# Kernel tuning notes

Hardware: AMD Instinct MI355X
Metric: run time of the kernel (lower is better)

## Reference

```python
import jax, jax.numpy as jnp
import numpy as np

NR_HEADS = 8


def segment_softmax(scores, indices, num_segments):
    # numerically stable softmax within each segment
    seg_max = jax.ops.segment_max(scores, indices, num_segments=num_segments)
    e = jnp.exp(scores - seg_max[indices])
    denom = jax.ops.segment_sum(e, indices, num_segments=num_segments)
    return e / denom[indices]


def setup_inputs() -> dict:
    key = jax.random.key(0)
    ks = jax.random.split(key, 10)
    n_ast, d, n_cfg = 500000, 128, 32768
    H, combined = NR_HEADS, 128
    w_scale = 1.0 / np.sqrt(d)
    return {
        "ast_nodes_encodings": jax.random.normal(ks[0], (n_ast, d), jnp.float32),
        "Wq": jax.random.normal(ks[1], (H, d, d), jnp.float32) * w_scale,
        "bq": jnp.zeros((H, d), jnp.float32),
        "Wk": jax.random.normal(ks[2], (H, d, d), jnp.float32) * w_scale,
        "bk": jnp.zeros((H, d), jnp.float32),
        "Wo": jax.random.normal(ks[3], (H * d, combined), jnp.float32) * (1.0 / np.sqrt(H * d)),
        "bo": jnp.zeros((combined,), jnp.float32),
        "ast_key": jax.random.randint(ks[4], (n_ast,), 0, n_ast, jnp.int32),
        "ast_value": jax.random.randint(ks[5], (n_ast,), 0, n_cfg, jnp.int32),
        "pdg_key": jnp.arange(n_cfg, dtype=jnp.int32),
        "pdg_value": jax.random.randint(ks[6], (n_cfg,), 0, n_ast, jnp.int32),
        "nr_cfg_nodes": n_cfg,
    }


def reference(ast_nodes_encodings, Wq, bq, Wk, bk, Wo, bo,
              ast_key, ast_value, pdg_key, pdg_value, nr_cfg_nodes):
    N = int(nr_cfg_nodes)
    d = ast_nodes_encodings.shape[1]
    inv_sqrt_d = 1.0 / np.sqrt(d)

    # Build per-PDG-node attention queries: gather sub-AST root encodings, scatter into [N, d]
    root_encodings = ast_nodes_encodings[pdg_value]                   # [N_map, d]
    attn_queries = jnp.zeros((N, d), ast_nodes_encodings.dtype).at[pdg_key].set(root_encodings)

    # Gather scattered inputs (one row per AST node assigned to a PDG node)
    values = ast_nodes_encodings[ast_key]                              # [E, d]
    indices = ast_value                                                # [E]

    # Multi-head scatter attention (ScatterCombiner with combining_method='attn')
    head_outs = []
    for h in range(NR_HEADS):  # small fixed head count; avoids [E, H, d] intermediates
        q = attn_queries @ Wq[h] + bq[h]                               # [N, d]
        k = values @ Wk[h] + bk[h]                                     # [E, d]
        scores = jnp.sum(q[indices] * k, axis=-1) * inv_sqrt_d         # [E]
        probs = segment_softmax(scores, indices, N)                    # [E]
        head_outs.append(jax.ops.segment_sum(probs[:, None] * values, indices, num_segments=N))

    combined = jnp.concatenate(head_outs, axis=-1) @ Wo + bo           # [N, combined_dim]
    return combined
```

## Files before the change

kernel.cpp:

```cpp
#include <hip/hip_runtime.h>
#include <hip/hip_bf16.h>
#include <cstdint>

typedef __hip_bfloat16 bf16;
typedef unsigned int uint;
typedef unsigned short ushort;

#define DEVI __device__ __forceinline__

DEVI float blo(uint u){ return __uint_as_float(u << 16); }
DEVI float bhi(uint u){ return __uint_as_float(u & 0xffff0000u); }
DEVI ushort f2b(float x){ uint u = __float_as_uint(x); uint r = (u + 0x7fffu + ((u >> 16) & 1u)) >> 16; return (ushort)r; }
DEVI uint pack2(float a, float b){ return (uint)f2b(a) | ((uint)f2b(b) << 16); }
DEVI float b2f(ushort h){ return __uint_as_float((uint)h << 16); }

typedef short bf16x8 __attribute__((ext_vector_type(8)));
typedef float f32x4  __attribute__((ext_vector_type(4)));

DEVI float row16_sum(float x){
  int y;
  y = __builtin_amdgcn_update_dpp(0, __float_as_int(x), 0x121, 0xF, 0xF, true); x += __int_as_float(y);
  y = __builtin_amdgcn_update_dpp(0, __float_as_int(x), 0x122, 0xF, 0xF, true); x += __int_as_float(y);
  y = __builtin_amdgcn_update_dpp(0, __float_as_int(x), 0x124, 0xF, 0xF, true); x += __int_as_float(y);
  y = __builtin_amdgcn_update_dpp(0, __float_as_int(x), 0x128, 0xF, 0xF, true); x += __int_as_float(y);
  return x;
}

__global__ __launch_bounds__(256) void build_M(const float* __restrict__ Wq, const float* __restrict__ Wk,
                                               float* __restrict__ Mb){
  __shared__ float WkL[128*33];
  __shared__ float WqL[16*33];
  const int t = threadIdx.x;
  const int h = blockIdx.x >> 3, pg = blockIdx.x & 7, p0 = pg*16;
  const float* wk = Wk + (size_t)h*16384;
  const float* wq = Wq + ((size_t)h*128 + p0)*128;
  const int m = t & 127, half = t >> 7;
  float acc[8] = {0,0,0,0,0,0,0,0};
  for (int jc = 0; jc < 4; ++jc){
    __syncthreads();
    #pragma unroll
    for (int i = 0; i < 4; ++i){
      int g = t + 256*i;
      int mm = g >> 3, j0 = (g & 7)*4;
      float4 v = *(const float4*)(wk + mm*128 + jc*32 + j0);
      float* d = &WkL[mm*33 + j0];
      d[0] = v.x; d[1] = v.y; d[2] = v.z; d[3] = v.w;
    }
    {
      int e = t*2;
      int pr = e >> 5, jj = e & 31;
      float2 v = *(const float2*)(wq + pr*128 + jc*32 + jj);
      WqL[pr*33 + jj] = v.x; WqL[pr*33 + jj + 1] = v.y;
    }
    __syncthreads();
    for (int j = 0; j < 32; ++j){
      float wkv = WkL[m*33 + j];
      #pragma unroll
      for (int r = 0; r < 8; ++r)
        acc[r] = fmaf(WqL[(half*8 + r)*33 + j], wkv, acc[r]);
    }
  }
  #pragma unroll
  for (int r = 0; r < 8; ++r)
    Mb[(size_t)(p0 + half*8 + r)*1024 + h*128 + m] = acc[r];
}

__global__ void build_bias(const float* __restrict__ Wq, const float* __restrict__ Wk,
                           const float* __restrict__ bq, const float* __restrict__ bk,
                           float* __restrict__ cvec, float* __restrict__ uvec, float* __restrict__ sv){
  int h = blockIdx.x, m = threadIdx.x;
  const float* wkr = Wk + ((size_t)h*128 + m)*128;
  const float* wqr = Wq + ((size_t)h*128 + m)*128;
  const float* bqr = bq + h*128;
  const float* bkr = bk + h*128;
  float c = 0.f, u = 0.f;
  for (int j = 0; j < 128; ++j){
    c = fmaf(wkr[j], bqr[j], c);
    u = fmaf(wqr[j], bkr[j], u);
  }
  cvec[h*128 + m] = c;
  uvec[h*128 + m] = u;
  if (m == 0){
    float s = 0.f;
    for (int j = 0; j < 128; ++j) s = fmaf(bqr[j], bkr[j], s);
    sv[h] = s;
  }
}

__global__ void scatter_aq(const int* __restrict__ pk, const int* __restrict__ pv,
                           const float* __restrict__ ast, float* __restrict__ aq,
                           ushort* __restrict__ aqh, ushort* __restrict__ aql, int n_map){
  int i = blockIdx.x;
  if (i >= n_map) return;
  int k = pk[i], src = pv[i];
  int lane = threadIdx.x;
  float2 v = *(const float2*)(ast + (size_t)src*128 + 2*lane);
  *(float2*)(aq + (size_t)k*128 + 2*lane) = v;
  ushort h0 = f2b(v.x), h1 = f2b(v.y);
  ushort l0 = f2b(v.x - b2f(h0)), l1 = f2b(v.y - b2f(h1));
  *(uint*)(aqh + (size_t)k*128 + 2*lane) = (uint)h0 | ((uint)h1 << 16);
  *(uint*)(aql + (size_t)k*128 + 2*lane) = (uint)l0 | ((uint)l1 << 16);
}

__global__ void frag_pack(const float* __restrict__ S, uint4* __restrict__ D, int C, int ctn){
  const int b = blockIdx.x;
  const int ks = b / ctn, ct = b - ks*ctn;
  const int l = threadIdx.x;
  const int kb = ks*32 + (l >> 4)*8;
  const int c  = ct*16 + (l & 15);
  ushort hi[8], lo[8];
  #pragma unroll
  for (int j = 0; j < 8; ++j){
    float wv = S[(size_t)(kb + j)*C + c];
    ushort hh = f2b(wv);
    hi[j] = hh;
    lo[j] = f2b(wv - b2f(hh));
  }
  uint4 H, L;
  H.x = (uint)hi[0] | ((uint)hi[1] << 16);
  H.y = (uint)hi[2] | ((uint)hi[3] << 16);
  H.z = (uint)hi[4] | ((uint)hi[5] << 16);
  H.w = (uint)hi[6] | ((uint)hi[7] << 16);
  L.x = (uint)lo[0] | ((uint)lo[1] << 16);
  L.y = (uint)lo[2] | ((uint)lo[3] << 16);
  L.z = (uint)lo[4] | ((uint)lo[5] << 16);
  L.w = (uint)lo[6] | ((uint)lo[7] << 16);
  D[((size_t)b*2 + 0)*64 + l] = H;
  D[((size_t)b*2 + 1)*64 + l] = L;
}

__global__ __launch_bounds__(256, 1) void qt_mfma(const ushort* __restrict__ aqh, const ushort* __restrict__ aql,
                                                  const uint4* __restrict__ Mp, const float* __restrict__ cvec,
                                                  bf16* __restrict__ qt, int N){
  const int l = threadIdx.x & 63, w = threadIdx.x >> 6;
  const int lr = l & 15, lk = l >> 4;
  const int r0 = blockIdx.x*128 + w*32;
  int ra = r0 + lr;      if (ra > N-1) ra = N-1;
  int rb = r0 + 16 + lr; if (rb > N-1) rb = N-1;

  bf16x8 Ah0[4], Al0[4], Ah1[4], Al1[4];
  #pragma unroll
  for (int ks = 0; ks < 4; ++ks){
    Ah0[ks] = *(const bf16x8*)(aqh + (size_t)ra*128 + lk*8 + ks*32);
    Al0[ks] = *(const bf16x8*)(aql + (size_t)ra*128 + lk*8 + ks*32);
    Ah1[ks] = *(const bf16x8*)(aqh + (size_t)rb*128 + lk*8 + ks*32);
    Al1[ks] = *(const bf16x8*)(aql + (size_t)rb*128 + lk*8 + ks*32);
  }
  const uint4* pw = Mp + l;

  bf16x8 Ba[8], Bb[8];
  auto LDB = [&](int ct, bf16x8* B){
    #pragma unroll
    for (int ks = 0; ks < 4; ++ks){
      const uint4* q = pw + ((size_t)(ks*64 + ct)*2)*64;
      B[ks*2]   = *(const bf16x8*)q;
      B[ks*2+1] = *(const bf16x8*)(q + 64);
    }
  };
  auto DO = [&](int ct, bf16x8* B){
    f32x4 a0 = {0.f,0.f,0.f,0.f}, a1 = {0.f,0.f,0.f,0.f};
    #pragma unroll
    for (int ks = 0; ks < 4; ++ks){
      a0 = __builtin_amdgcn_mfma_f32_16x16x32_bf16(Ah0[ks], B[2*ks],   a0, 0, 0, 0);
      a1 = __builtin_amdgcn_mfma_f32_16x16x32_bf16(Ah1[ks], B[2*ks],   a1, 0, 0, 0);
      a0 = __builtin_amdgcn_mfma_f32_16x16x32_bf16(Al0[ks], B[2*ks],   a0, 0, 0, 0);
      a1 = __builtin_amdgcn_mfma_f32_16x16x32_bf16(Al1[ks], B[2*ks],   a1, 0, 0, 0);
      a0 = __builtin_amdgcn_mfma_f32_16x16x32_bf16(Ah0[ks], B[2*ks+1], a0, 0, 0, 0);
      a1 = __builtin_amdgcn_mfma_f32_16x16x32_bf16(Ah1[ks], B[2*ks+1], a1, 0, 0, 0);
    }
    const int cc = ct*16 + lr;
    const float bv = cvec[cc];
    #pragma unroll
    for (int i = 0; i < 4; ++i){
      int rr0 = r0 + lk*4 + i;
      if (rr0 < N) ((ushort*)qt)[(size_t)rr0*1024 + cc] = f2b(a0[i] + bv);
      int rr1 = r0 + 16 + lk*4 + i;
      if (rr1 < N) ((ushort*)qt)[(size_t)rr1*1024 + cc] = f2b(a1[i] + bv);
    }
  };

  LDB(0, Ba);
  for (int ct = 0; ct < 64; ct += 2){
    LDB(ct + 1, Bb);
    DO(ct, Ba);
    if (ct + 2 < 64) LDB(ct + 2, Ba);
    DO(ct + 1, Bb);
  }
}

__global__ void qb_kernel(const float* __restrict__ aq, const float* __restrict__ uvec,
                          const float* __restrict__ sv, float* __restrict__ qb){
  int n = blockIdx.x, lane = threadIdx.x;
  int h = lane >> 3, g = lane & 7;
  const float* ar = aq + (size_t)n*128 + g*16;
  const float* ur = uvec + h*128 + g*16;
  float dot = 0.f;
  #pragma unroll
  for (int k = 0; k < 16; ++k) dot = fmaf(ar[k], ur[k], dot);
  dot += __shfl_xor(dot, 1);
  dot += __shfl_xor(dot, 2);
  dot += __shfl_xor(dot, 4);
  if (g == 0) qb[(size_t)n*8 + h] = dot + sv[h];
}

__global__ void count_edges(const int* __restrict__ av, int* __restrict__ counts, int E){
  int e = blockIdx.x*256 + threadIdx.x;
  if (e < E) atomicAdd(&counts[av[e]], 1);
}

__global__ void scan_offsets(const int* __restrict__ counts, int* __restrict__ offsets, int N){
  __shared__ int pa[1024];
  __shared__ int pb[1024];
  int t = threadIdx.x;
  int CH = (N + 1023) >> 10;
  int b = t*CH, e = b + CH;
  if (b > N) b = N;
  if (e > N) e = N;
  int s = 0;
  for (int i = b; i < e; ++i) s += counts[i];
  pa[t] = s;
  __syncthreads();
  int* src = pa; int* dst = pb;
  for (int off = 1; off < 1024; off <<= 1){
    int v = src[t];
    if (t >= off) v += src[t - off];
    __syncthreads();
    dst[t] = v;
    __syncthreads();
    int* tmp = src; src = dst; dst = tmp;
  }
  int run = src[t] - s;
  for (int i = b; i < e; ++i){ offsets[i] = run; run += counts[i]; }
  if (t == 1023) offsets[N] = src[1023];
}

__global__ void fill_edges(const int* __restrict__ av, const int* __restrict__ akey,
                           const int* __restrict__ offsets, int* __restrict__ cursor,
                           int* __restrict__ ridx, int E){
  int e = blockIdx.x*256 + threadIdx.x;
  if (e < E){
    int seg = av[e];
    int pos = offsets[seg] + atomicAdd(&cursor[seg], 1);
    ridx[pos] = akey[e];
  }
}

__global__ __launch_bounds__(256) void seg_attn(
    const bf16* __restrict__ qt, const float* __restrict__ qb,
    const int* __restrict__ offsets, const int* __restrict__ ridx,
    const float* __restrict__ ast, bf16* __restrict__ ho, int N)
{
  const int wid  = threadIdx.x >> 6;
  const int lane = threadIdx.x & 63;
  const int n = blockIdx.x*4 + wid;
  if (n >= N) return;
  const int beg = __builtin_amdgcn_readfirstlane(offsets[n]);
  const int end = __builtin_amdgcn_readfirstlane(offsets[n+1]);
  const int deg = end - beg;
  const int grp = lane >> 4, d4 = lane & 15;
  const int h0 = 2*grp, h1 = 2*grp + 1;

  const ushort* qtp = (const ushort*)qt + (size_t)n*1024 + d4*8;
  const uint4 Qa = *(const uint4*)(qtp + h0*128);
  const uint4 Qb = *(const uint4*)(qtp + h1*128);
  const float4 q0lo = make_float4(blo(Qa.x), bhi(Qa.x), blo(Qa.y), bhi(Qa.y));
  const float4 q0hi = make_float4(blo(Qa.z), bhi(Qa.z), blo(Qa.w), bhi(Qa.w));
  const float4 q1lo = make_float4(blo(Qb.x), bhi(Qb.x), blo(Qb.y), bhi(Qb.y));
  const float4 q1hi = make_float4(blo(Qb.z), bhi(Qb.z), blo(Qb.w), bhi(Qb.w));
  const float SC = 0.12751744886681336f;
  const float qs0 = qb[(size_t)n*8 + h0] * SC;
  const float qs1 = qb[(size_t)n*8 + h1] * SC;

  const int* rp = ridx + beg;

  float den0 = 0.f, den1 = 0.f;
  float4 x0lo = make_float4(0,0,0,0), x0hi = x0lo, x1lo = x0lo, x1hi = x0lo;

  if (deg > 0){
#define LOADP(Pa0, Pa1, Pb0, Pb1, base) do { \
    int iA = (base) < deg ? (base) : deg-1; \
    int iB = (base)+1 < deg ? (base)+1 : deg-1; \
    const float4* pA = (const float4*)(ast + (size_t)rp[iA]*128 + d4*8); \
    const float4* pB = (const float4*)(ast + (size_t)rp[iB]*128 + d4*8); \
    Pa0 = pA[0]; Pa1 = pA[1]; Pb0 = pB[0]; Pb1 = pB[1]; } while(0)

#define C1(A0, A1) do { \
    float s0, s1; \
    s0 = A0.x*q0lo.x; s0 = fmaf(A0.y, q0lo.y, s0); s0 = fmaf(A0.z, q0lo.z, s0); s0 = fmaf(A0.w, q0lo.w, s0); \
    s0 = fmaf(A1.x, q0hi.x, s0); s0 = fmaf(A1.y, q0hi.y, s0); s0 = fmaf(A1.z, q0hi.z, s0); s0 = fmaf(A1.w, q0hi.w, s0); \
    s1 = A0.x*q1lo.x; s1 = fmaf(A0.y, q1lo.y, s1); s1 = fmaf(A0.z, q1lo.z, s1); s1 = fmaf(A0.w, q1lo.w, s1); \
    s1 = fmaf(A1.x, q1hi.x, s1); s1 = fmaf(A1.y, q1hi.y, s1); s1 = fmaf(A1.z, q1hi.z, s1); s1 = fmaf(A1.w, q1hi.w, s1); \
    s0 = row16_sum(s0); s1 = row16_sum(s1); \
    const float p0 = exp2f(fmaf(s0, SC, qs0)); \
    const float p1 = exp2f(fmaf(s1, SC, qs1)); \
    den0 += p0; den1 += p1; \
    x0lo.x = fmaf(p0, A0.x, x0lo.x); x0lo.y = fmaf(p0, A0.y, x0lo.y); \
    x0lo.z = fmaf(p0, A0.z, x0lo.z); x0lo.w = fmaf(p0, A0.w, x0lo.w); \
    x0hi.x = fmaf(p0, A1.x, x0hi.x); x0hi.y = fmaf(p0, A1.y, x0hi.y); \
    x0hi.z = fmaf(p0, A1.z, x0hi.z); x0hi.w = fmaf(p0, A1.w, x0hi.w); \
    x1lo.x = fmaf(p1, A0.x, x1lo.x); x1lo.y = fmaf(p1, A0.y, x1lo.y); \
    x1lo.z = fmaf(p1, A0.z, x1lo.z); x1lo.w = fmaf(p1, A0.w, x1lo.w); \
    x1hi.x = fmaf(p1, A1.x, x1hi.x); x1hi.y = fmaf(p1, A1.y, x1hi.y); \
    x1hi.z = fmaf(p1, A1.z, x1hi.z); x1hi.w = fmaf(p1, A1.w, x1hi.w); \
  } while(0)

    float4 P0a0, P0a1, P0b0, P0b1;
    float4 P1a0, P1a1, P1b0, P1b1;
    float4 P2a0, P2a1, P2b0, P2b1;
    LOADP(P0a0, P0a1, P0b0, P0b1, 0);
    LOADP(P1a0, P1a1, P1b0, P1b1, 2);
    LOADP(P2a0, P2a1, P2b0, P2b1, 4);
    int e = 0;
    for (; e + 5 < deg; e += 6){
      C1(P0a0, P0a1); C1(P0b0, P0b1); LOADP(P0a0, P0a1, P0b0, P0b1, e + 6);
      C1(P1a0, P1a1); C1(P1b0, P1b1); LOADP(P1a0, P1a1, P1b0, P1b1, e + 8);
      C1(P2a0, P2a1); C1(P2b0, P2b1); LOADP(P2a0, P2a1, P2b0, P2b1, e + 10);
    }
    const int t = deg - e;
    if (t >= 1) C1(P0a0, P0a1);
    if (t >= 2) C1(P0b0, P0b1);
    if (t >= 3) C1(P1a0, P1a1);
    if (t >= 4) C1(P1b0, P1b1);
    if (t >= 5) C1(P2a0, P2a1);
    if (t >= 6) C1(P2b0, P2b1);
#undef C1
#undef LOADP
  }
  const float r0v = (deg > 0) ? (1.f / den0) : 0.f;
  const float r1v = (deg > 0) ? (1.f / den1) : 0.f;

  uint4 o0, o1;
  o0.x = pack2(x0lo.x*r0v, x0lo.y*r0v); o0.y = pack2(x0lo.z*r0v, x0lo.w*r0v);
  o0.z = pack2(x0hi.x*r0v, x0hi.y*r0v); o0.w = pack2(x0hi.z*r0v, x0hi.w*r0v);
  o1.x = pack2(x1lo.x*r1v, x1lo.y*r1v); o1.y = pack2(x1lo.z*r1v, x1lo.w*r1v);
  o1.z = pack2(x1hi.x*r1v, x1hi.y*r1v); o1.w = pack2(x1hi.z*r1v, x1hi.w*r1v);
  ushort* hb = (ushort*)ho + (size_t)n*1024 + d4*8;
  *(uint4*)(hb + h0*128) = o0;
  *(uint4*)(hb + h1*128) = o1;
}

__global__ __launch_bounds__(256, 1) void out_mfma(const bf16* __restrict__ ho, const uint4* __restrict__ Wp,
                                                   const float* __restrict__ bo, float* __restrict__ out, int N){
  const int l = threadIdx.x & 63, w = threadIdx.x >> 6;
  const int lr = l & 15, lk = l >> 4;
  const int r0 = blockIdx.x*128 + w*32;
  int ra = r0 + lr;      if (ra > N-1) ra = N-1;
  int rb = r0 + 16 + lr; if (rb > N-1) rb = N-1;
  const bf16* pa = ho + (size_t)ra*1024 + lk*8;
  const bf16* pb = ho + (size_t)rb*1024 + lk*8;
  const uint4* pw = Wp + l;

  f32x4 acc[2][8];
  #pragma unroll
  for (int i = 0; i < 2; ++i)
    #pragma unroll
    for (int c = 0; c < 8; ++c)
      #pragma unroll
      for (int j = 0; j < 4; ++j) acc[i][c][j] = 0.f;

  bf16x8 Aa[2], Ab[2], Ba[16], Bb[16];

  auto LD = [&](int ks, bf16x8* A, bf16x8* B){
    A[0] = *(const bf16x8*)(pa + ks*32);
    A[1] = *(const bf16x8*)(pb + ks*32);
    const uint4* q = pw + (size_t)ks*1024;
    #pragma unroll
    for (int u = 0; u < 16; ++u) B[u] = *(const bf16x8*)(q + (size_t)u*64);
  };
  auto MM = [&](bf16x8* A, bf16x8* B){
    #pragma unroll
    for (int c = 0; c < 8; ++c){
      acc[0][c] = __builtin_amdgcn_mfma_f32_16x16x32_bf16(A[0], B[2*c],   acc[0][c], 0, 0, 0);
      acc[1][c] = __builtin_amdgcn_mfma_f32_16x16x32_bf16(A[1], B[2*c],   acc[1][c], 0, 0, 0);
      acc[0][c] = __builtin_amdgcn_mfma_f32_16x16x32_bf16(A[0], B[2*c+1], acc[0][c], 0, 0, 0);
      acc[1][c] = __builtin_amdgcn_mfma_f32_16x16x32_bf16(A[1], B[2*c+1], acc[1][c], 0, 0, 0);
    }
  };

  LD(0, Aa, Ba);
  for (int ks = 0; ks < 32; ks += 2){
    LD(ks + 1, Ab, Bb);
    MM(Aa, Ba);
    if (ks + 2 < 32) LD(ks + 2, Aa, Ba);
    MM(Ab, Bb);
  }

  #pragma unroll
  for (int c = 0; c < 8; ++c){
    float bv = bo[c*16 + lr];
    #pragma unroll
    for (int rt = 0; rt < 2; ++rt){
      #pragma unroll
      for (int i = 0; i < 4; ++i){
        int rr = r0 + rt*16 + lk*4 + i;
        if (rr < N) out[(size_t)rr*128 + c*16 + lr] = acc[rt][c][i] + bv;
      }
    }
  }
}

extern "C" void kernel_launch(void* const* d_in, const int* in_sizes, int n_in,
                              void* d_out, int out_size, void* d_ws, size_t ws_size,
                              hipStream_t stream) {
  const float* ast = (const float*)d_in[0];
  const float* Wq  = (const float*)d_in[1];
  const float* bq  = (const float*)d_in[2];
  const float* Wk  = (const float*)d_in[3];
  const float* bk  = (const float*)d_in[4];
  const float* Wo  = (const float*)d_in[5];
  const float* bo  = (const float*)d_in[6];
  const int* ast_key   = (const int*)d_in[7];
  const int* ast_value = (const int*)d_in[8];
  const int* pdg_key   = (const int*)d_in[9];
  const int* pdg_value = (const int*)d_in[10];
  const int E     = in_sizes[7];
  const int n_map = in_sizes[9];
  const int N     = out_size / 128;
  float* out = (float*)d_out;

  char* w = (char*)d_ws;
  auto carve = [&](size_t bytes)->char*{
    char* p = w; w += (bytes + 255) & ~size_t(255); return p;
  };
  bf16*  qt      = (bf16*) carve((size_t)N*1024*2);
  float* aq      = (float*)carve((size_t)N*128*4);
  float* Mb      = (float*)carve((size_t)128*1024*4);
  float* cvec    = (float*)carve(1024*4);
  float* uvec    = (float*)carve(1024*4);
  float* sv      = (float*)carve(8*4);
  float* qb      = (float*)carve((size_t)N*8*4);
  int*   counts  = (int*)  carve((size_t)N*4);
  int*   offsets = (int*)  carve((size_t)(N+1)*4);
  int*   cursor  = (int*)  carve((size_t)N*4);
  int*   ridx    = (int*)  carve((size_t)E*4);
  bf16*  ho      = (bf16*) carve((size_t)N*1024*2);
  uint4* Wp      = (uint4*)carve((size_t)256*2*64*16);
  ushort* aqh    = (ushort*)carve((size_t)N*128*2);
  ushort* aql    = (ushort*)carve((size_t)N*128*2);
  uint4* Mp      = (uint4*)carve((size_t)256*2*64*16);
  (void)ws_size; (void)n_in;

  hipMemsetAsync(aq,     0, (size_t)N*128*4, stream);
  hipMemsetAsync(aqh,    0, (size_t)N*128*2, stream);
  hipMemsetAsync(aql,    0, (size_t)N*128*2, stream);
  hipMemsetAsync(counts, 0, (size_t)N*4, stream);
  hipMemsetAsync(cursor, 0, (size_t)N*4, stream);

  build_M   <<<64, 256, 0, stream>>>(Wq, Wk, Mb);
  build_bias<<<8, 128, 0, stream>>>(Wq, Wk, bq, bk, cvec, uvec, sv);
  frag_pack <<<256, 64, 0, stream>>>(Wo, Wp, 128, 8);
  scatter_aq<<<n_map, 64, 0, stream>>>(pdg_key, pdg_value, ast, aq, aqh, aql, n_map);
  frag_pack <<<256, 64, 0, stream>>>(Mb, Mp, 1024, 64);
  qt_mfma   <<<(N + 127)/128, 256, 0, stream>>>(aqh, aql, Mp, cvec, qt, N);
  qb_kernel <<<N, 64, 0, stream>>>(aq, uvec, sv, qb);
  count_edges<<<(E + 255)/256, 256, 0, stream>>>(ast_value, counts, E);
  scan_offsets<<<1, 1024, 0, stream>>>(counts, offsets, N);
  fill_edges<<<(E + 255)/256, 256, 0, stream>>>(ast_value, ast_key, offsets, cursor, ridx, E);
  seg_attn  <<<(N + 3)/4, 256, 0, stream>>>(qt, qb, offsets, ridx, ast, ho, N);
  out_mfma  <<<(N + 127)/128, 256, 0, stream>>>(ho, Wp, bo, out, N);
}
```

Measured before the change: 756.7 us.

## Merge preprocessing kernels into fused launches and prefetch edge indices via readlane

Folds build_M, build_bias, Wo packing, edge counting, scan, Mp packing, scatter, qb and fill_edges into three block-range-dispatched kernels, and merges the memsets by making buffers contiguous. This cuts the launch count and lets independent small jobs run concurrently. The segment attention loop now loads up to 64 row indices per wave at once and broadcasts them with readlane, using 4-deep prefetch instead of per-edge scalar index loads. The scan drops from 1024 to 256 threads, so each thread handles a longer serial chunk.

```diff
diff --git a/kernel.cpp b/kernel.cpp
--- a/kernel.cpp
+++ b/kernel.cpp
@@ -26,86 +26,8 @@
   return x;
 }
 
-__global__ __launch_bounds__(256) void build_M(const float* __restrict__ Wq, const float* __restrict__ Wk,
-                                               float* __restrict__ Mb){
-  __shared__ float WkL[128*33];
-  __shared__ float WqL[16*33];
-  const int t = threadIdx.x;
-  const int h = blockIdx.x >> 3, pg = blockIdx.x & 7, p0 = pg*16;
-  const float* wk = Wk + (size_t)h*16384;
-  const float* wq = Wq + ((size_t)h*128 + p0)*128;
-  const int m = t & 127, half = t >> 7;
-  float acc[8] = {0,0,0,0,0,0,0,0};
-  for (int jc = 0; jc < 4; ++jc){
-    __syncthreads();
-    #pragma unroll
-    for (int i = 0; i < 4; ++i){
-      int g = t + 256*i;
-      int mm = g >> 3, j0 = (g & 7)*4;
-      float4 v = *(const float4*)(wk + mm*128 + jc*32 + j0);
-      float* d = &WkL[mm*33 + j0];
-      d[0] = v.x; d[1] = v.y; d[2] = v.z; d[3] = v.w;
-    }
-    {
-      int e = t*2;
-      int pr = e >> 5, jj = e & 31;
-      float2 v = *(const float2*)(wq + pr*128 + jc*32 + jj);
-      WqL[pr*33 + jj] = v.x; WqL[pr*33 + jj + 1] = v.y;
-    }
-    __syncthreads();
-    for (int j = 0; j < 32; ++j){
-      float wkv = WkL[m*33 + j];
-      #pragma unroll
-      for (int r = 0; r < 8; ++r)
-        acc[r] = fmaf(WqL[(half*8 + r)*33 + j], wkv, acc[r]);
-    }
-  }
-  #pragma unroll
-  for (int r = 0; r < 8; ++r)
-    Mb[(size_t)(p0 + half*8 + r)*1024 + h*128 + m] = acc[r];
-}
-
-__global__ void build_bias(const float* __restrict__ Wq, const float* __restrict__ Wk,
-                           const float* __restrict__ bq, const float* __restrict__ bk,
-                           float* __restrict__ cvec, float* __restrict__ uvec, float* __restrict__ sv){
-  int h = blockIdx.x, m = threadIdx.x;
-  const float* wkr = Wk + ((size_t)h*128 + m)*128;
-  const float* wqr = Wq + ((size_t)h*128 + m)*128;
-  const float* bqr = bq + h*128;
-  const float* bkr = bk + h*128;
-  float c = 0.f, u = 0.f;
-  for (int j = 0; j < 128; ++j){
-    c = fmaf(wkr[j], bqr[j], c);
-    u = fmaf(wqr[j], bkr[j], u);
-  }
-  cvec[h*128 + m] = c;
-  uvec[h*128 + m] = u;
-  if (m == 0){
-    float s = 0.f;
-    for (int j = 0; j < 128; ++j) s = fmaf(bqr[j], bkr[j], s);
-    sv[h] = s;
-  }
-}
-
-__global__ void scatter_aq(const int* __restrict__ pk, const int* __restrict__ pv,
-                           const float* __restrict__ ast, float* __restrict__ aq,
-                           ushort* __restrict__ aqh, ushort* __restrict__ aql, int n_map){
-  int i = blockIdx.x;
-  if (i >= n_map) return;
-  int k = pk[i], src = pv[i];
-  int lane = threadIdx.x;
-  float2 v = *(const float2*)(ast + (size_t)src*128 + 2*lane);
-  *(float2*)(aq + (size_t)k*128 + 2*lane) = v;
-  ushort h0 = f2b(v.x), h1 = f2b(v.y);
-  ushort l0 = f2b(v.x - b2f(h0)), l1 = f2b(v.y - b2f(h1));
-  *(uint*)(aqh + (size_t)k*128 + 2*lane) = (uint)h0 | ((uint)h1 << 16);
-  *(uint*)(aql + (size_t)k*128 + 2*lane) = (uint)l0 | ((uint)l1 << 16);
-}
-
-__global__ void frag_pack(const float* __restrict__ S, uint4* __restrict__ D, int C, int ctn){
-  const int b = blockIdx.x;
+DEVI void frag_pack_body(const float* __restrict__ S, uint4* __restrict__ D, int C, int ctn, int b, int l){
   const int ks = b / ctn, ct = b - ks*ctn;
-  const int l = threadIdx.x;
   const int kb = ks*32 + (l >> 4)*8;
   const int c  = ct*16 + (l & 15);
   ushort hi[8], lo[8];
@@ -129,6 +51,158 @@
   D[((size_t)b*2 + 1)*64 + l] = L;
 }
 
+__global__ __launch_bounds__(256) void prep1(
+    const float* __restrict__ Wq, const float* __restrict__ Wk,
+    const float* __restrict__ bq, const float* __restrict__ bk,
+    const float* __restrict__ Wo, const int* __restrict__ av,
+    float* __restrict__ Mb, float* __restrict__ cvec, float* __restrict__ uvec,
+    float* __restrict__ sv, uint4* __restrict__ Wp, int* __restrict__ counts, int E)
+{
+  __shared__ float WkL[128*33];
+  __shared__ float WqL[16*33];
+  const int b = blockIdx.x, t = threadIdx.x;
+  if (b < 64){
+    const int h = b >> 3, pg = b & 7, p0 = pg*16;
+    const float* wk = Wk + (size_t)h*16384;
+    const float* wq = Wq + ((size_t)h*128 + p0)*128;
+    const int m = t & 127, half = t >> 7;
+    float acc[8] = {0,0,0,0,0,0,0,0};
+    for (int jc = 0; jc < 4; ++jc){
+      __syncthreads();
+      #pragma unroll
+      for (int i = 0; i < 4; ++i){
+        int g = t + 256*i;
+        int mm = g >> 3, j0 = (g & 7)*4;
+        float4 v = *(const float4*)(wk + mm*128 + jc*32 + j0);
+        float* d = &WkL[mm*33 + j0];
+        d[0] = v.x; d[1] = v.y; d[2] = v.z; d[3] = v.w;
+      }
+      {
+        int e = t*2;
+        int pr = e >> 5, jj = e & 31;
+        float2 v = *(const float2*)(wq + pr*128 + jc*32 + jj);
+        WqL[pr*33 + jj] = v.x; WqL[pr*33 + jj + 1] = v.y;
+      }
+      __syncthreads();
+      for (int j = 0; j < 32; ++j){
+        float wkv = WkL[m*33 + j];
+        #pragma unroll
+        for (int r = 0; r < 8; ++r)
+          acc[r] = fmaf(WqL[(half*8 + r)*33 + j], wkv, acc[r]);
+      }
+    }
+    #pragma unroll
+    for (int r = 0; r < 8; ++r)
+      Mb[(size_t)(p0 + half*8 + r)*1024 + h*128 + m] = acc[r];
+  } else if (b < 72){
+    if (t < 128){
+      int h = b - 64, m = t;
+      const float* wkr = Wk + ((size_t)h*128 + m)*128;
+      const float* wqr = Wq + ((size_t)h*128 + m)*128;
+      const float* bqr = bq + h*128;
+      const float* bkr = bk + h*128;
+      float c = 0.f, u = 0.f;
+      for (int j = 0; j < 128; ++j){
+        c = fmaf(wkr[j], bqr[j], c);
+        u = fmaf(wqr[j], bkr[j], u);
+      }
+      cvec[h*128 + m] = c;
+      uvec[h*128 + m] = u;
+      if (m == 0){
+        float s = 0.f;
+        for (int j = 0; j < 128; ++j) s = fmaf(bqr[j], bkr[j], s);
+        sv[h] = s;
+      }
+    }
+  } else if (b < 328){
+    if (t < 64) frag_pack_body(Wo, Wp, 128, 8, b - 72, t);
+  } else {
+    int e = (b - 328)*256 + t;
+    if (e < E) atomicAdd(&counts[av[e]], 1);
+  }
+}
+
+__global__ __launch_bounds__(256) void prep2(
+    const int* __restrict__ counts, int* __restrict__ offsets, int N,
+    const float* __restrict__ Mb, uint4* __restrict__ Mp,
+    const int* __restrict__ pk, const int* __restrict__ pv,
+    const float* __restrict__ ast, float* __restrict__ aq,
+    ushort* __restrict__ aqh, ushort* __restrict__ aql, int n_map)
+{
+  __shared__ int pa[256];
+  __shared__ int pb[256];
+  const int b = blockIdx.x, t = threadIdx.x;
+  if (b == 0){
+    const int CH = (N + 255) >> 8;
+    int b0 = t*CH, e0 = b0 + CH;
+    if (b0 > N) b0 = N;
+    if (e0 > N) e0 = N;
+    int s = 0;
+    for (int i = b0; i < e0; ++i) s += counts[i];
+    pa[t] = s;
+    __syncthreads();
+    int* src = pa; int* dst = pb;
+    for (int off = 1; off < 256; off <<= 1){
+      int v = src[t];
+      if (t >= off) v += src[t - off];
+      __syncthreads();
+      dst[t] = v;
+      __syncthreads();
+      int* tmp = src; src = dst; dst = tmp;
+    }
+    int run = src[t] - s;
+    for (int i = b0; i < e0; ++i){ offsets[i] = run; run += counts[i]; }
+    if (t == 255) offsets[N] = src[255];
+  } else if (b < 257){
+    if (t < 64) frag_pack_body(Mb, Mp, 1024, 64, b - 1, t);
+  } else {
+    int i = (b - 257)*4 + (t >> 6);
+    int lane = t & 63;
+    if (i < n_map){
+      int k = pk[i], src = pv[i];
+      float2 v = *(const float2*)(ast + (size_t)src*128 + 2*lane);
+      *(float2*)(aq + (size_t)k*128 + 2*lane) = v;
+      ushort h0 = f2b(v.x), h1 = f2b(v.y);
+      ushort l0 = f2b(v.x - b2f(h0)), l1 = f2b(v.y - b2f(h1));
+      *(uint*)(aqh + (size_t)k*128 + 2*lane) = (uint)h0 | ((uint)h1 << 16);
+      *(uint*)(aql + (size_t)k*128 + 2*lane) = (uint)l0 | ((uint)l1 << 16);
+    }
+  }
+}
+
+__global__ __launch_bounds__(256) void prep3(
+    const float* __restrict__ aq, const float* __restrict__ uvec, const float* __restrict__ sv,
+    float* __restrict__ qb, const int* __restrict__ av, const int* __restrict__ akey,
+    const int* __restrict__ offsets, int* __restrict__ cursor, int* __restrict__ ridx,
+    int N, int E)
+{
+  const int b = blockIdx.x, t = threadIdx.x;
+  const int nqb = (N + 3) >> 2;
+  if (b < nqb){
+    int n = b*4 + (t >> 6);
+    int lane = t & 63;
+    if (n < N){
+      int h = lane >> 3, g = lane & 7;
+      const float* ar = aq + (size_t)n*128 + g*16;
+      const float* ur = uvec + h*128 + g*16;
+      float dot = 0.f;
+      #pragma unroll
+      for (int k = 0; k < 16; ++k) dot = fmaf(ar[k], ur[k], dot);
+      dot += __shfl_xor(dot, 1);
+      dot += __shfl_xor(dot, 2);
+      dot += __shfl_xor(dot, 4);
+      if (g == 0) qb[(size_t)n*8 + h] = dot + sv[h];
+    }
+  } else {
+    int e = (b - nqb)*256 + t;
+    if (e < E){
+      int seg = av[e];
+      int pos = offsets[seg] + atomicAdd(&cursor[seg], 1);
+      ridx[pos] = akey[e];
+    }
+  }
+}
+
 __global__ __launch_bounds__(256, 1) void qt_mfma(const ushort* __restrict__ aqh, const ushort* __restrict__ aql,
                                                   const uint4* __restrict__ Mp, const float* __restrict__ cvec,
                                                   bf16* __restrict__ qt, int N){
@@ -188,64 +262,7 @@
   }
 }
 
-__global__ void qb_kernel(const float* __restrict__ aq, const float* __restrict__ uvec,
-                          const float* __restrict__ sv, float* __restrict__ qb){
-  int n = blockIdx.x, lane = threadIdx.x;
-  int h = lane >> 3, g = lane & 7;
-  const float* ar = aq + (size_t)n*128 + g*16;
-  const float* ur = uvec + h*128 + g*16;
-  float dot = 0.f;
-  #pragma unroll
-  for (int k = 0; k < 16; ++k) dot = fmaf(ar[k], ur[k], dot);
-  dot += __shfl_xor(dot, 1);
-  dot += __shfl_xor(dot, 2);
-  dot += __shfl_xor(dot, 4);
-  if (g == 0) qb[(size_t)n*8 + h] = dot + sv[h];
-}
-
-__global__ void count_edges(const int* __restrict__ av, int* __restrict__ counts, int E){
-  int e = blockIdx.x*256 + threadIdx.x;
-  if (e < E) atomicAdd(&counts[av[e]], 1);
-}
-
-__global__ void scan_offsets(const int* __restrict__ counts, int* __restrict__ offsets, int N){
-  __shared__ int pa[1024];
-  __shared__ int pb[1024];
-  int t = threadIdx.x;
-  int CH = (N + 1023) >> 10;
-  int b = t*CH, e = b + CH;
-  if (b > N) b = N;
-  if (e > N) e = N;
-  int s = 0;
-  for (int i = b; i < e; ++i) s += counts[i];
-  pa[t] = s;
-  __syncthreads();
-  int* src = pa; int* dst = pb;
-  for (int off = 1; off < 1024; off <<= 1){
-    int v = src[t];
-    if (t >= off) v += src[t - off];
-    __syncthreads();
-    dst[t] = v;
-    __syncthreads();
-    int* tmp = src; src = dst; dst = tmp;
-  }
-  int run = src[t] - s;
-  for (int i = b; i < e; ++i){ offsets[i] = run; run += counts[i]; }
-  if (t == 1023) offsets[N] = src[1023];
-}
-
-__global__ void fill_edges(const int* __restrict__ av, const int* __restrict__ akey,
-                           const int* __restrict__ offsets, int* __restrict__ cursor,
-                           int* __restrict__ ridx, int E){
-  int e = blockIdx.x*256 + threadIdx.x;
-  if (e < E){
-    int seg = av[e];
-    int pos = offsets[seg] + atomicAdd(&cursor[seg], 1);
-    ridx[pos] = akey[e];
-  }
-}
-
-__global__ __launch_bounds__(256) void seg_attn(
+__global__ __launch_bounds__(256, 4) void seg_attn(
     const bf16* __restrict__ qt, const float* __restrict__ qb,
     const int* __restrict__ offsets, const int* __restrict__ ridx,
     const float* __restrict__ ast, bf16* __restrict__ ho, int N)
@@ -259,30 +276,33 @@
   const int deg = end - beg;
   const int grp = lane >> 4, d4 = lane & 15;
   const int h0 = 2*grp, h1 = 2*grp + 1;
+  const int vo = d4*2;
+  const int* rp = ridx + beg;
+
+  int idx0 = lane < deg ? lane : (deg - 1);
+  int rlist0 = (deg > 0) ? rp[idx0] : 0;
 
   const ushort* qtp = (const ushort*)qt + (size_t)n*1024 + d4*8;
   const uint4 Qa = *(const uint4*)(qtp + h0*128);
   const uint4 Qb = *(const uint4*)(qtp + h1*128);
+  const float SC = 0.12751744886681336f;
+  const float qs0 = qb[(size_t)n*8 + h0] * SC;
+  const float qs1 = qb[(size_t)n*8 + h1] * SC;
   const float4 q0lo = make_float4(blo(Qa.x), bhi(Qa.x), blo(Qa.y), bhi(Qa.y));
   const float4 q0hi = make_float4(blo(Qa.z), bhi(Qa.z), blo(Qa.w), bhi(Qa.w));
   const float4 q1lo = make_float4(blo(Qb.x), bhi(Qb.x), blo(Qb.y), bhi(Qb.y));
   const float4 q1hi = make_float4(blo(Qb.z), bhi(Qb.z), blo(Qb.w), bhi(Qb.w));
-  const float SC = 0.12751744886681336f;
-  const float qs0 = qb[(size_t)n*8 + h0] * SC;
-  const float qs1 = qb[(size_t)n*8 + h1] * SC;
-
-  const int* rp = ridx + beg;
 
   float den0 = 0.f, den1 = 0.f;
   float4 x0lo = make_float4(0,0,0,0), x0hi = x0lo, x1lo = x0lo, x1hi = x0lo;
 
-  if (deg > 0){
-#define LOADP(Pa0, Pa1, Pb0, Pb1, base) do { \
-    int iA = (base) < deg ? (base) : deg-1; \
-    int iB = (base)+1 < deg ? (base)+1 : deg-1; \
-    const float4* pA = (const float4*)(ast + (size_t)rp[iA]*128 + d4*8); \
-    const float4* pB = (const float4*)(ast + (size_t)rp[iB]*128 + d4*8); \
-    Pa0 = pA[0]; Pa1 = pA[1]; Pb0 = pB[0]; Pb1 = pB[1]; } while(0)
+#define ISSUE(Pa0, Pa1, Pb0, Pb1, pidx) do { \
+    int pi_ = (pidx); pi_ = pi_ > 31 ? 31 : pi_; \
+    int rA_ = __builtin_amdgcn_readlane(rlist, 2*pi_); \
+    int rB_ = __builtin_amdgcn_readlane(rlist, 2*pi_ + 1); \
+    const float4* pA_ = (const float4*)(ast + (size_t)(uint)rA_*128) + vo; \
+    const float4* pB_ = (const float4*)(ast + (size_t)(uint)rB_*128) + vo; \
+    Pa0 = pA_[0]; Pa1 = pA_[1]; Pb0 = pB_[0]; Pb1 = pB_[1]; } while(0)
 
 #define C1(A0, A1) do { \
     float s0, s1; \
@@ -304,28 +324,45 @@
     x1hi.z = fmaf(p1, A1.z, x1hi.z); x1hi.w = fmaf(p1, A1.w, x1hi.w); \
   } while(0)
 
+  for (int c0 = 0; c0 < deg; c0 += 64){
+    int ecnt = deg - c0; if (ecnt > 64) ecnt = 64;
+    const int np = (ecnt + 1) >> 1;
+    int rlist;
+    if (c0 == 0){
+      rlist = rlist0;
+    } else {
+      int ii = c0 + lane; if (ii >= deg) ii = deg - 1;
+      rlist = rp[ii];
+    }
     float4 P0a0, P0a1, P0b0, P0b1;
     float4 P1a0, P1a1, P1b0, P1b1;
     float4 P2a0, P2a1, P2b0, P2b1;
-    LOADP(P0a0, P0a1, P0b0, P0b1, 0);
-    LOADP(P1a0, P1a1, P1b0, P1b1, 2);
-    LOADP(P2a0, P2a1, P2b0, P2b1, 4);
-    int e = 0;
-    for (; e + 5 < deg; e += 6){
-      C1(P0a0, P0a1); C1(P0b0, P0b1); LOADP(P0a0, P0a1, P0b0, P0b1, e + 6);
-      C1(P1a0, P1a1); C1(P1b0, P1b1); LOADP(P1a0, P1a1, P1b0, P1b1, e + 8);
-      C1(P2a0, P2a1); C1(P2b0, P2b1); LOADP(P2a0, P2a1, P2b0, P2b1, e + 10);
-    }
-    const int t = deg - e;
-    if (t >= 1) C1(P0a0, P0a1);
-    if (t >= 2) C1(P0b0, P0b1);
-    if (t >= 3) C1(P1a0, P1a1);
-    if (t >= 4) C1(P1b0, P1b1);
-    if (t >= 5) C1(P2a0, P2a1);
-    if (t >= 6) C1(P2b0, P2b1);
+    float4 P3a0, P3a1, P3b0, P3b1;
+    ISSUE(P0a0, P0a1, P0b0, P0b1, 0);
+    if (np > 1) ISSUE(P1a0, P1a1, P1b0, P1b1, 1);
+    if (np > 2) ISSUE(P2a0, P2a1, P2b0, P2b1, 2);
+    if (np > 3) ISSUE(P3a0, P3a1, P3b0, P3b1, 3);
+
+    int p = 0;
+    for (; p + 4 < np; p += 4){
+      C1(P0a0, P0a1); C1(P0b0, P0b1);
+      if (p + 4 < np) ISSUE(P0a0, P0a1, P0b0, P0b1, p + 4);
+      C1(P1a0, P1a1); C1(P1b0, P1b1);
+      if (p + 5 < np) ISSUE(P1a0, P1a1, P1b0, P1b1, p + 5);
+      C1(P2a0, P2a1); C1(P2b0, P2b1);
+      if (p + 6 < np) ISSUE(P2a0, P2a1, P2b0, P2b1, p + 6);
+      C1(P3a0, P3a1); C1(P3b0, P3b1);
+      if (p + 7 < np) ISSUE(P3a0, P3a1, P3b0, P3b1, p + 7);
+    }
+    const int rem = np - p;
+    {              C1(P0a0, P0a1); if (2*p + 1 < ecnt) C1(P0b0, P0b1); }
+    if (rem > 1){  C1(P1a0, P1a1); if (2*p + 3 < ecnt) C1(P1b0, P1b1); }
+    if (rem > 2){  C1(P2a0, P2a1); if (2*p + 5 < ecnt) C1(P2b0, P2b1); }
+    if (rem > 3){  C1(P3a0, P3a1); if (2*p + 7 < ecnt) C1(P3b0, P3b1); }
+  }
 #undef C1
-#undef LOADP
-  }
+#undef ISSUE
+
   const float r0v = (deg > 0) ? (1.f / den0) : 0.f;
   const float r1v = (deg > 0) ? (1.f / den1) : 0.f;
 
@@ -424,38 +461,33 @@
   };
   bf16*  qt      = (bf16*) carve((size_t)N*1024*2);
   float* aq      = (float*)carve((size_t)N*128*4);
+  ushort* aqh    = (ushort*)carve((size_t)N*128*2);
+  ushort* aql    = (ushort*)carve((size_t)N*128*2);
   float* Mb      = (float*)carve((size_t)128*1024*4);
   float* cvec    = (float*)carve(1024*4);
   float* uvec    = (float*)carve(1024*4);
   float* sv      = (float*)carve(8*4);
   float* qb      = (float*)carve((size_t)N*8*4);
   int*   counts  = (int*)  carve((size_t)N*4);
+  int*   cursor  = (int*)  carve((size_t)N*4);
   int*   offsets = (int*)  carve((size_t)(N+1)*4);
-  int*   cursor  = (int*)  carve((size_t)N*4);
   int*   ridx    = (int*)  carve((size_t)E*4);
   bf16*  ho      = (bf16*) carve((size_t)N*1024*2);
   uint4* Wp      = (uint4*)carve((size_t)256*2*64*16);
-  ushort* aqh    = (ushort*)carve((size_t)N*128*2);
-  ushort* aql    = (ushort*)carve((size_t)N*128*2);
   uint4* Mp      = (uint4*)carve((size_t)256*2*64*16);
   (void)ws_size; (void)n_in;
 
-  hipMemsetAsync(aq,     0, (size_t)N*128*4, stream);
-  hipMemsetAsync(aqh,    0, (size_t)N*128*2, stream);
-  hipMemsetAsync(aql,    0, (size_t)N*128*2, stream);
-  hipMemsetAsync(counts, 0, (size_t)N*4, stream);
-  hipMemsetAsync(cursor, 0, (size_t)N*4, stream);
-
-  build_M   <<<64, 256, 0, stream>>>(Wq, Wk, Mb);
-  build_bias<<<8, 128, 0, stream>>>(Wq, Wk, bq, bk, cvec, uvec, sv);
-  frag_pack <<<256, 64, 0, stream>>>(Wo, Wp, 128, 8);
-  scatter_aq<<<n_map, 64, 0, stream>>>(pdg_key, pdg_value, ast, aq, aqh, aql, n_map);
-  frag_pack <<<256, 64, 0, stream>>>(Mb, Mp, 1024, 64);
-  qt_mfma   <<<(N + 127)/128, 256, 0, stream>>>(aqh, aql, Mp, cvec, qt, N);
-  qb_kernel <<<N, 64, 0, stream>>>(aq, uvec, sv, qb);
-  count_edges<<<(E + 255)/256, 256, 0, stream>>>(ast_value, counts, E);
-  scan_offsets<<<1, 1024, 0, stream>>>(counts, offsets, N);
-  fill_edges<<<(E + 255)/256, 256, 0, stream>>>(ast_value, ast_key, offsets, cursor, ridx, E);
-  seg_attn  <<<(N + 3)/4, 256, 0, stream>>>(qt, qb, offsets, ridx, ast, ho, N);
-  out_mfma  <<<(N + 127)/128, 256, 0, stream>>>(ho, Wp, bo, out, N);
-}
+  hipMemsetAsync(aq,     0, (size_t)N*128*8, stream);
+  hipMemsetAsync(counts, 0, (size_t)N*8, stream);
+
+  const int nb_cnt  = (E + 255)/256;
+  const int nb_sca  = (n_map + 3)/4;
+  const int nb_qb   = (N + 3)/4;
+
+  prep1<<<328 + nb_cnt, 256, 0, stream>>>(Wq, Wk, bq, bk, Wo, ast_value, Mb, cvec, uvec, sv, Wp, counts, E);
+  prep2<<<257 + nb_sca, 256, 0, stream>>>(counts, offsets, N, Mb, Mp, pdg_key, pdg_value, ast, aq, aqh, aql, n_map);
+  qt_mfma<<<(N + 127)/128, 256, 0, stream>>>(aqh, aql, Mp, cvec, qt, N);
+  prep3<<<nb_qb + nb_cnt, 256, 0, stream>>>(aq, uvec, sv, qb, ast_value, ast_key, offsets, cursor, ridx, N, E);
+  seg_attn<<<(N + 3)/4, 256, 0, stream>>>(qt, qb, offsets, ridx, ast, ho, N);
+  out_mfma<<<(N + 127)/128, 256, 0, stream>>>(ho, Wp, bo, out, N);
+}
```

Result: slower. 1.274 ms (+68.3%).
